# Performance work log

Hardware: AMD Instinct MI355X
Metric: run time of the kernel (lower is better)

## Reference

```python
import jax, jax.numpy as jnp
import numpy as np

N_GLIMPSES = 3
GS = 64          # glimpse_size
IN_C = 3         # input_channels
B, H, W = 64, 512, 512


def get_glimpses(image, loc):
    """Multi-scale glimpse extraction (tf.image.extract_glimpse, centered+normalized)
    followed by antialiased bicubic resize to GS x GS, concatenated on channels."""
    b, h, w, c = image.shape
    max_size = GS * 2 ** (N_GLIMPSES - 1)
    padded = jnp.pad(image, ((0, 0), (max_size, max_size), (max_size, max_size), (0, 0)))
    hp, wp = h + 2 * max_size, w + 2 * max_size
    # normalized+centered offsets: (-1,-1)=upper-left, (1,1)=lower-right of padded image
    center = (loc + 1.0) * 0.5 * jnp.array([hp, wp], dtype=jnp.float32)  # (y, x) per batch
    glimpses = []
    for i in range(N_GLIMPSES):
        s = GS * 2 ** i  # current crop size (python int, static)
        tl = jnp.round(center - 0.5 * s).astype(jnp.int32)
        tl = jnp.clip(tl, 0, jnp.array([hp - s, wp - s], dtype=jnp.int32))

        def slice_one(img, yx):
            return jax.lax.dynamic_slice(img, (yx[0], yx[1], 0), (s, s, c))

        g = jax.vmap(slice_one)(padded, tl)                      # [B, s, s, C]
        g = jax.image.resize(g, (b, GS, GS, c), method='cubic')  # antialiased bicubic
        glimpses.append(g)
    return jnp.concatenate(glimpses, axis=-1)  # [B, GS, GS, N_GLIMPSES*C]


def setup_inputs() -> dict:
    key = jax.random.key(0)
    ks = jax.random.split(key, 10)
    image = jax.random.uniform(ks[0], (B, H, W, IN_C), dtype=jnp.float32)
    loc = jax.random.uniform(ks[1], (B, 2), dtype=jnp.float32, minval=-1.0, maxval=1.0)
    cg = N_GLIMPSES * IN_C
    # conv1_g: full-kernel (GS x GS) valid conv -> 1x1x128
    Wg = jax.random.normal(ks[2], (GS, GS, cg, 128), dtype=jnp.float32) * (1.0 / np.sqrt(GS * GS * cg))
    bg = jnp.zeros((128,), jnp.float32)
    # conv1_l: 1x1 conv on loc [B,1,1,2]
    Wl = jax.random.normal(ks[3], (2, 128), dtype=jnp.float32) * (1.0 / np.sqrt(2.0))
    bl = jnp.zeros((128,), jnp.float32)
    # out: 1x1 conv 128 -> 256
    Wo = jax.random.normal(ks[4], (128, 256), dtype=jnp.float32) * (1.0 / np.sqrt(128.0))
    bo = jnp.zeros((256,), jnp.float32)
    return {"image": image, "loc": loc, "Wg": Wg, "bg": bg, "Wl": Wl, "bl": bl, "Wo": Wo, "bo": bo}


def reference(image, loc, Wg, bg, Wl, bl, Wo, bo):
    glimpses = get_glimpses(image, loc)  # [B, GS, GS, N_GLIMPSES*IN_C]
    # conv1_g with kernel == glimpse size and VALID padding == dense contraction over hwc
    x1 = jax.nn.relu(jnp.einsum('bhwc,hwck->bk', glimpses, Wg) + bg)  # [B,128]
    x2 = jax.nn.relu(loc @ Wl + bl)                                   # [B,128]
    out = jax.nn.relu((x1 + x2) @ Wo + bo)                            # [B,256]
    return out
```

## Files before the change

### kernel.cpp

```cpp
#include <hip/hip_runtime.h>
#include <hip/hip_bf16.h>

#define IMG_H 512
#define IMG_W 512
#define PAD   256
#define HP    1024
#define BATCH 64
#define KTOT  36864
#define KTILE 96
#define NTILES 384
#define TBLK  1152

typedef __attribute__((ext_vector_type(8))) short short8;
typedef __attribute__((ext_vector_type(4))) float f32x4;

__device__ __forceinline__ float keys_cubic(float x) {
  if (x >= 2.0f) return 0.0f;
  if (x >= 1.0f) return ((-0.5f * x + 2.5f) * x - 4.0f) * x + 2.0f;
  return ((1.5f * x - 2.5f) * x) * x + 1.0f;
}

__device__ __forceinline__ int iclamp(int v, int lo, int hi) {
  return min(max(v, lo), hi);
}
__device__ __forceinline__ unsigned short f2bits(float f) {
  __hip_bfloat16 h = __float2bfloat16(f);
  unsigned short s;
  __builtin_memcpy(&s, &h, 2);
  return s;
}

__global__ __launch_bounds__(256) void prep_kernel(
    const float* __restrict__ Wg, unsigned short* __restrict__ Wt,
    float* __restrict__ WT) {
  if (blockIdx.x == TBLK) {
    const int t = threadIdx.x;
    if (t < 64) {
      float sx = ((float)t + 0.5f) * 2.0f - 0.5f;
      int ix0 = (int)ceilf(sx - 4.0f);
      float ws = 0.0f;
#pragma unroll
      for (int tap = 0; tap < 8; ++tap) {
        int i = ix0 + tap;
        float w = (i >= 0 && i < 128) ? keys_cubic(fabsf(sx - (float)i) * 0.5f) : 0.0f;
        WT[t * 9 + tap] = w;
        ws += w;
      }
      WT[t * 9 + 8] = ws;
    } else if (t < 128) {
      const int xo = t - 64;
      float sx = ((float)xo + 0.5f) * 4.0f - 0.5f;
      int ix0 = (int)ceilf(sx - 8.0f);
      float ws = 0.0f;
#pragma unroll
      for (int tap = 0; tap < 16; ++tap) {
        int i = ix0 + tap;
        float w = (i >= 0 && i < 256) ? keys_cubic(fabsf(sx - (float)i) * 0.25f) : 0.0f;
        WT[576 + xo * 17 + tap] = w;
        ws += w;
      }
      WT[576 + xo * 17 + 16] = ws;
    }
    return;
  }

  __shared__ float T[64][68];
  const int tid = threadIdx.x;
  const int kt  = (blockIdx.x % 576) * 64;
  const int nt0 = (blockIdx.x / 576) * 64;
  {
    const int r = tid >> 4, nc = tid & 15;
#pragma unroll
    for (int kk = 0; kk < 4; ++kk) {
      const int k = kk * 16 + r;
      const float4 v = *(const float4*)(Wg + (size_t)(kt + k) * 128 + nt0 + nc * 4);
      *(float4*)(&T[k][nc * 4]) = v;
    }
  }
  __syncthreads();
#pragma unroll
  for (int it = 0; it < 2; ++it) {
    const int item = tid + 256 * it;
    const int n = item & 63, ko = item >> 6;
    short8 o;
#pragma unroll
    for (int j = 0; j < 8; ++j) o[j] = (short)f2bits(T[ko * 8 + j][n]);
    *(short8*)(Wt + (size_t)(nt0 + n) * KTOT + kt + ko * 8) = o;
  }
}

__global__ __launch_bounds__(256) void glimpse_kernel(
    const float* __restrict__ img, const float* __restrict__ loc,
    const float* __restrict__ WT, unsigned short* __restrict__ G) {
  __shared__ __align__(16) float Ws[1664];
  __shared__ float wv1n[8], wv2n[16];
  __shared__ float tmp1[384];
  __shared__ float tmp2[768];
  const int y   = blockIdx.x & 63;
  const int b   = blockIdx.x >> 6;
  const int tid = threadIdx.x;

  {
    const float4* src = (const float4*)WT;
    float4* dst = (float4*)Ws;
    for (int e = tid; e < 416; e += 256) dst[e] = src[e];
  }

  const float cy = (loc[2 * b] + 1.0f) * 0.5f * 1024.0f;
  const float cx = (loc[2 * b + 1] + 1.0f) * 0.5f * 1024.0f;
  const int tly0 = iclamp((int)rintf(cy - 32.0f), 0, HP - 64);
  const int tlx0 = iclamp((int)rintf(cx - 32.0f), 0, HP - 64);
  const int tly1 = iclamp((int)rintf(cy - 64.0f), 0, HP - 128);
  const int tlx1 = iclamp((int)rintf(cx - 64.0f), 0, HP - 128);
  const int tly2 = iclamp((int)rintf(cy - 128.0f), 0, HP - 256);
  const int tlx2 = iclamp((int)rintf(cx - 128.0f), 0, HP - 256);
  const float* imb = img + (size_t)b * (IMG_H * IMG_W * 3);
  unsigned short* Grow = G + ((size_t)b * 64 + y) * (64 * 9);

  if (tid < 192) {
    int x = tid / 3, c = tid - 3 * (tid / 3);
    int py = tly0 + y - PAD, px = tlx0 + x - PAD;
    float v = 0.0f;
    if ((unsigned)py < (unsigned)IMG_H && (unsigned)px < (unsigned)IMG_W)
      v = imb[(py * IMG_W + px) * 3 + c];
    Grow[x * 9 + c] = f2bits(v);
  }
  __syncthreads();

  if (tid < 8) {
    wv1n[tid] = Ws[y * 9 + tid] * (1.0f / Ws[y * 9 + 8]);
  } else if (tid >= 64 && tid < 80) {
    const int t = tid - 64;
    wv2n[t] = Ws[576 + y * 17 + t] * (1.0f / Ws[576 + y * 17 + 16]);
  }
  __syncthreads();

  const float sy1 = ((float)y + 0.5f) * 2.0f - 0.5f;
  const int iy0_1 = (int)ceilf(sy1 - 4.0f);
  const float sy2 = ((float)y + 0.5f) * 4.0f - 0.5f;
  const int iy0_2 = (int)ceilf(sy2 - 8.0f);
  float rw1[8], rw2[16];
#pragma unroll
  for (int t = 0; t < 8; ++t) rw1[t] = wv1n[t];
#pragma unroll
  for (int t = 0; t < 16; ++t) rw2[t] = wv2n[t];

  for (int e = tid; e < 384; e += 256) {
    int x = e / 3, c = e - 3 * (e / 3);
    int px = tlx1 - PAD + x;
    float a = 0.0f;
    if ((unsigned)px < (unsigned)IMG_W) {
      const float* colp = imb + (px * 3 + c);
#pragma unroll
      for (int t = 0; t < 8; ++t) {
        int py = tly1 + iy0_1 + t - PAD;
        if ((unsigned)py < (unsigned)IMG_H)
          a = fmaf(rw1[t], colp[py * (IMG_W * 3)], a);
      }
    }
    tmp1[e] = a;
  }
  for (int e = tid; e < 768; e += 256) {
    int x = e / 3, c = e - 3 * (e / 3);
    int px = tlx2 - PAD + x;
    float a = 0.0f;
    if ((unsigned)px < (unsigned)IMG_W) {
      const float* colp = imb + (px * 3 + c);
#pragma unroll
      for (int t = 0; t < 16; ++t) {
        int py = tly2 + iy0_2 + t - PAD;
        if ((unsigned)py < (unsigned)IMG_H)
          a = fmaf(rw2[t], colp[py * (IMG_W * 3)], a);
      }
    }
    tmp2[e] = a;
  }
  __syncthreads();

  for (int o = tid; o < 384; o += 256) {
    int oo = (o >= 192) ? o - 192 : o;
    int xo = oo / 3, c = oo - 3 * xo;
    if (o < 192) {
      const float* wr = Ws + xo * 9;
      float sx  = ((float)xo + 0.5f) * 2.0f - 0.5f;
      int   ix0 = (int)ceilf(sx - 4.0f);
      float a = 0.0f;
#pragma unroll
      for (int t = 0; t < 8; ++t) {
        int ic = iclamp(ix0 + t, 0, 127);
        a = fmaf(wr[t], tmp1[ic * 3 + c], a);
      }
      Grow[xo * 9 + 3 + c] = f2bits(a / wr[8]);
    } else {
      const float* wr = Ws + 576 + xo * 17;
      float sx  = ((float)xo + 0.5f) * 4.0f - 0.5f;
      int   ix0 = (int)ceilf(sx - 8.0f);
      float a = 0.0f;
#pragma unroll
      for (int t = 0; t < 16; ++t) {
        int ic = iclamp(ix0 + t, 0, 255);
        a = fmaf(wr[t], tmp2[ic * 3 + c], a);
      }
      Grow[xo * 9 + 6 + c] = f2bits(a / wr[16]);
    }
  }
}

__global__ __launch_bounds__(256) void gemm_kernel(
    const unsigned short* __restrict__ G, const unsigned short* __restrict__ Wt,
    float* __restrict__ partials) {
  const int tid  = threadIdx.x;
  const int tile = blockIdx.x;
  const int kt   = tile * KTILE;
  const int lane = tid & 63;
  const int wv   = tid >> 6;
  const int ln   = lane & 15;
  const int q    = lane >> 4;
  const int nb   = wv * 32 + ln;

  f32x4 acc[4][2];
#pragma unroll
  for (int mt = 0; mt < 4; ++mt)
#pragma unroll
    for (int nt = 0; nt < 2; ++nt) {
      acc[mt][nt][0] = 0.f; acc[mt][nt][1] = 0.f;
      acc[mt][nt][2] = 0.f; acc[mt][nt][3] = 0.f;
    }

  const unsigned short* Ab = G + kt + q * 8;
  const unsigned short* Bb = Wt + kt + q * 8;

#pragma unroll
  for (int s = 0; s < KTILE / 32; ++s) {
    short8 af[4];
#pragma unroll
    for (int mt = 0; mt < 4; ++mt)
      af[mt] = *(const short8*)(Ab + (size_t)(mt * 16 + ln) * KTOT + s * 32);
    short8 bf[2];
#pragma unroll
    for (int nt = 0; nt < 2; ++nt)
      bf[nt] = *(const short8*)(Bb + (size_t)(nb + nt * 16) * KTOT + s * 32);
#pragma unroll
    for (int mt = 0; mt < 4; ++mt)
#pragma unroll
      for (int nt = 0; nt < 2; ++nt)
        acc[mt][nt] = __builtin_amdgcn_mfma_f32_16x16x32_bf16(
            af[mt], bf[nt], acc[mt][nt], 0, 0, 0);
  }

#pragma unroll
  for (int mt = 0; mt < 4; ++mt)
#pragma unroll
    for (int nt = 0; nt < 2; ++nt)
#pragma unroll
      for (int i = 0; i < 4; ++i) {
        const int row = mt * 16 + q * 4 + i;
        const int col = nb + nt * 16;
        partials[((size_t)row * NTILES + tile) * 128 + col] = acc[mt][nt][i];
      }
}

__global__ __launch_bounds__(512) void finalize_kernel(
    const float* __restrict__ partials, const float* __restrict__ loc,
    const float* __restrict__ bg, const float* __restrict__ Wl,
    const float* __restrict__ bl, const float* __restrict__ Wo,
    const float* __restrict__ bo, float* __restrict__ out) {
  const int b   = blockIdx.x;
  const int tid = threadIdx.x;

  const float4* base = (const float4*)(partials + (size_t)b * NTILES * 128);
  float4 acc = make_float4(0.f, 0.f, 0.f, 0.f);
#pragma unroll 8
  for (int i = 0; i < 24; ++i) {
    float4 v = base[(size_t)i * 512 + tid];
    acc.x += v.x; acc.y += v.y; acc.z += v.z; acc.w += v.w;
  }

  __shared__ float red[16][128];
  __shared__ float h[128];
  {
    float* r = &red[tid >> 5][(tid & 31) * 4];
    r[0] = acc.x; r[1] = acc.y; r[2] = acc.z; r[3] = acc.w;
  }
  __syncthreads();
  if (tid < 128) {
    float ss = 0.0f;
#pragma unroll
    for (int g = 0; g < 16; ++g) ss += red[g][tid];
    float x1 = fmaxf(ss + bg[tid], 0.0f);
    float x2 = fmaxf(fmaf(loc[2 * b], Wl[tid],
                          fmaf(loc[2 * b + 1], Wl[128 + tid], bl[tid])),
                     0.0f);
    h[tid] = x1 + x2;
  }
  __syncthreads();
  if (tid < 256) {
    const int n = tid;
    float a = bo[n];
#pragma unroll 8
    for (int kk = 0; kk < 128; ++kk) a = fmaf(h[kk], Wo[kk * 256 + n], a);
    out[(size_t)b * 256 + n] = fmaxf(a, 0.0f);
  }
}

extern "C" void kernel_launch(void* const* d_in, const int* in_sizes, int n_in,
                              void* d_out, int out_size, void* d_ws, size_t ws_size,
                              hipStream_t stream) {
  const float* img = (const float*)d_in[0];
  const float* loc = (const float*)d_in[1];
  const float* Wg  = (const float*)d_in[2];
  const float* bg  = (const float*)d_in[3];
  const float* Wl  = (const float*)d_in[4];
  const float* bl  = (const float*)d_in[5];
  const float* Wo  = (const float*)d_in[6];
  const float* bo  = (const float*)d_in[7];
  float* out = (float*)d_out;

  char* ws = (char*)d_ws;
  unsigned short* G = (unsigned short*)ws;
  float* partials   = (float*)(ws + 4718592);
  unsigned short* Wt = (unsigned short*)(ws + 4718592 + 12582912);
  float* WTbl       = (float*)(ws + 4718592 + 12582912 + 9437184);

  prep_kernel<<<TBLK + 1, 256, 0, stream>>>(Wg, Wt, WTbl);
  glimpse_kernel<<<BATCH * 64, 256, 0, stream>>>(img, loc, WTbl, G);
  gemm_kernel<<<NTILES, 256, 0, stream>>>(G, Wt, partials);
  finalize_kernel<<<BATCH, 512, 0, stream>>>(partials, loc, bg, Wl, bl, Wo, bo, out);
}
```

Measured before the change: 317.5 us.

## Merge weight prep and glimpse kernels, retile GEMM split-K across N halves

Fuses the weight transpose/bf16 conversion and glimpse extraction into one launch. Each glimpse block now computes the bicubic tap weights itself instead of reading a precomputed table, which removes a kernel launch and the dependency between the two stages. The GEMM switches to 192-wide K tiles with each block covering one 64-column half of N, giving the same block count with fewer partials. Finalize reduces those partials using 1024 threads. The cost is some redundant weight-table math in every glimpse block and a larger per-block K loop.

```diff
diff --git a/kernel.cpp b/kernel.cpp
--- a/kernel.cpp
+++ b/kernel.cpp
@@ -7,9 +7,10 @@
 #define HP    1024
 #define BATCH 64
 #define KTOT  36864
-#define KTILE 96
-#define NTILES 384
+#define KTILE 192
+#define NKT   192
 #define TBLK  1152
+#define GBLK  4096
 
 typedef __attribute__((ext_vector_type(8))) short short8;
 typedef __attribute__((ext_vector_type(4))) float f32x4;
@@ -30,80 +31,75 @@
   return s;
 }
 
-__global__ __launch_bounds__(256) void prep_kernel(
+__global__ __launch_bounds__(256) void combo_kernel(
+    const float* __restrict__ img, const float* __restrict__ loc,
     const float* __restrict__ Wg, unsigned short* __restrict__ Wt,
-    float* __restrict__ WT) {
-  if (blockIdx.x == TBLK) {
-    const int t = threadIdx.x;
-    if (t < 64) {
-      float sx = ((float)t + 0.5f) * 2.0f - 0.5f;
-      int ix0 = (int)ceilf(sx - 4.0f);
-      float ws = 0.0f;
-#pragma unroll
-      for (int tap = 0; tap < 8; ++tap) {
-        int i = ix0 + tap;
-        float w = (i >= 0 && i < 128) ? keys_cubic(fabsf(sx - (float)i) * 0.5f) : 0.0f;
-        WT[t * 9 + tap] = w;
-        ws += w;
-      }
-      WT[t * 9 + 8] = ws;
-    } else if (t < 128) {
-      const int xo = t - 64;
-      float sx = ((float)xo + 0.5f) * 4.0f - 0.5f;
-      int ix0 = (int)ceilf(sx - 8.0f);
-      float ws = 0.0f;
-#pragma unroll
-      for (int tap = 0; tap < 16; ++tap) {
-        int i = ix0 + tap;
-        float w = (i >= 0 && i < 256) ? keys_cubic(fabsf(sx - (float)i) * 0.25f) : 0.0f;
-        WT[576 + xo * 17 + tap] = w;
-        ws += w;
-      }
-      WT[576 + xo * 17 + 16] = ws;
+    unsigned short* __restrict__ G) {
+  __shared__ __align__(16) float smem[4352];
+  const int tid = threadIdx.x;
+
+  if (blockIdx.x < TBLK) {
+    float (*T)[68] = (float(*)[68])smem;
+    const int bid = blockIdx.x;
+    const int kt  = (bid % 576) * 64;
+    const int nt0 = (bid / 576) * 64;
+    {
+      const int r = tid >> 4, nc = tid & 15;
+#pragma unroll
+      for (int kk = 0; kk < 4; ++kk) {
+        const int k = kk * 16 + r;
+        const float4 v = *(const float4*)(Wg + (size_t)(kt + k) * 128 + nt0 + nc * 4);
+        *(float4*)(&T[k][nc * 4]) = v;
+      }
+    }
+    __syncthreads();
+#pragma unroll
+    for (int it = 0; it < 2; ++it) {
+      const int item = tid + 256 * it;
+      const int n = item & 63, ko = item >> 6;
+      short8 o;
+#pragma unroll
+      for (int j = 0; j < 8; ++j) o[j] = (short)f2bits(T[ko * 8 + j][n]);
+      *(short8*)(Wt + (size_t)(nt0 + n) * KTOT + kt + ko * 8) = o;
     }
     return;
   }
 
-  __shared__ float T[64][68];
-  const int tid = threadIdx.x;
-  const int kt  = (blockIdx.x % 576) * 64;
-  const int nt0 = (blockIdx.x / 576) * 64;
-  {
-    const int r = tid >> 4, nc = tid & 15;
-#pragma unroll
-    for (int kk = 0; kk < 4; ++kk) {
-      const int k = kk * 16 + r;
-      const float4 v = *(const float4*)(Wg + (size_t)(kt + k) * 128 + nt0 + nc * 4);
-      *(float4*)(&T[k][nc * 4]) = v;
-    }
-  }
-  __syncthreads();
-#pragma unroll
-  for (int it = 0; it < 2; ++it) {
-    const int item = tid + 256 * it;
-    const int n = item & 63, ko = item >> 6;
-    short8 o;
-#pragma unroll
-    for (int j = 0; j < 8; ++j) o[j] = (short)f2bits(T[ko * 8 + j][n]);
-    *(short8*)(Wt + (size_t)(nt0 + n) * KTOT + kt + ko * 8) = o;
-  }
-}
-
-__global__ __launch_bounds__(256) void glimpse_kernel(
-    const float* __restrict__ img, const float* __restrict__ loc,
-    const float* __restrict__ WT, unsigned short* __restrict__ G) {
-  __shared__ __align__(16) float Ws[1664];
-  __shared__ float wv1n[8], wv2n[16];
-  __shared__ float tmp1[384];
-  __shared__ float tmp2[768];
-  const int y   = blockIdx.x & 63;
-  const int b   = blockIdx.x >> 6;
-  const int tid = threadIdx.x;
-
-  {
-    const float4* src = (const float4*)WT;
-    float4* dst = (float4*)Ws;
-    for (int e = tid; e < 416; e += 256) dst[e] = src[e];
+  float* Ws   = smem;
+  float* tmp1 = smem + 1664;
+  float* tmp2 = smem + 2048;
+  float* wv1n = smem + 2816;
+  float* wv2n = smem + 2824;
+
+  const int bid = blockIdx.x - TBLK;
+  const int y   = bid & 63;
+  const int b   = bid >> 6;
+
+  if (tid < 64) {
+    float sx = ((float)tid + 0.5f) * 2.0f - 0.5f;
+    int ix0 = (int)ceilf(sx - 4.0f);
+    float ws = 0.0f;
+#pragma unroll
+    for (int tap = 0; tap < 8; ++tap) {
+      int i = ix0 + tap;
+      float w = (i >= 0 && i < 128) ? keys_cubic(fabsf(sx - (float)i) * 0.5f) : 0.0f;
+      Ws[tid * 9 + tap] = w;
+      ws += w;
+    }
+    Ws[tid * 9 + 8] = ws;
+  } else if (tid < 128) {
+    const int xo = tid - 64;
+    float sx = ((float)xo + 0.5f) * 4.0f - 0.5f;
+    int ix0 = (int)ceilf(sx - 8.0f);
+    float ws = 0.0f;
+#pragma unroll
+    for (int tap = 0; tap < 16; ++tap) {
+      int i = ix0 + tap;
+      float w = (i >= 0 && i < 256) ? keys_cubic(fabsf(sx - (float)i) * 0.25f) : 0.0f;
+      Ws[576 + xo * 17 + tap] = w;
+      ws += w;
+    }
+    Ws[576 + xo * 17 + 16] = ws;
   }
 
   const float cy = (loc[2 * b] + 1.0f) * 0.5f * 1024.0f;
@@ -209,26 +205,25 @@
 __global__ __launch_bounds__(256) void gemm_kernel(
     const unsigned short* __restrict__ G, const unsigned short* __restrict__ Wt,
     float* __restrict__ partials) {
-  const int tid  = threadIdx.x;
-  const int tile = blockIdx.x;
-  const int kt   = tile * KTILE;
-  const int lane = tid & 63;
-  const int wv   = tid >> 6;
-  const int ln   = lane & 15;
-  const int q    = lane >> 4;
-  const int nb   = wv * 32 + ln;
-
-  f32x4 acc[4][2];
-#pragma unroll
-  for (int mt = 0; mt < 4; ++mt)
-#pragma unroll
-    for (int nt = 0; nt < 2; ++nt) {
-      acc[mt][nt][0] = 0.f; acc[mt][nt][1] = 0.f;
-      acc[mt][nt][2] = 0.f; acc[mt][nt][3] = 0.f;
-    }
+  const int tid   = threadIdx.x;
+  const int bid   = blockIdx.x;
+  const int ktile = bid >> 1;
+  const int nh    = bid & 1;
+  const int kt    = ktile * KTILE;
+  const int lane  = tid & 63;
+  const int wv    = tid >> 6;
+  const int ln    = lane & 15;
+  const int q     = lane >> 4;
+  const int gcol  = nh * 64 + wv * 16 + ln;
+
+  f32x4 acc[4];
+#pragma unroll
+  for (int mt = 0; mt < 4; ++mt) {
+    acc[mt][0] = 0.f; acc[mt][1] = 0.f; acc[mt][2] = 0.f; acc[mt][3] = 0.f;
+  }
 
   const unsigned short* Ab = G + kt + q * 8;
-  const unsigned short* Bb = Wt + kt + q * 8;
+  const unsigned short* Bb = Wt + (size_t)gcol * KTOT + kt + q * 8;
 
 #pragma unroll
   for (int s = 0; s < KTILE / 32; ++s) {
@@ -236,31 +231,22 @@
 #pragma unroll
     for (int mt = 0; mt < 4; ++mt)
       af[mt] = *(const short8*)(Ab + (size_t)(mt * 16 + ln) * KTOT + s * 32);
-    short8 bf[2];
-#pragma unroll
-    for (int nt = 0; nt < 2; ++nt)
-      bf[nt] = *(const short8*)(Bb + (size_t)(nb + nt * 16) * KTOT + s * 32);
+    const short8 bf = *(const short8*)(Bb + s * 32);
 #pragma unroll
     for (int mt = 0; mt < 4; ++mt)
-#pragma unroll
-      for (int nt = 0; nt < 2; ++nt)
-        acc[mt][nt] = __builtin_amdgcn_mfma_f32_16x16x32_bf16(
-            af[mt], bf[nt], acc[mt][nt], 0, 0, 0);
+      acc[mt] = __builtin_amdgcn_mfma_f32_16x16x32_bf16(af[mt], bf, acc[mt], 0, 0, 0);
   }
 
 #pragma unroll
   for (int mt = 0; mt < 4; ++mt)
 #pragma unroll
-    for (int nt = 0; nt < 2; ++nt)
-#pragma unroll
-      for (int i = 0; i < 4; ++i) {
-        const int row = mt * 16 + q * 4 + i;
-        const int col = nb + nt * 16;
-        partials[((size_t)row * NTILES + tile) * 128 + col] = acc[mt][nt][i];
-      }
-}
-
-__global__ __launch_bounds__(512) void finalize_kernel(
+    for (int i = 0; i < 4; ++i) {
+      const int row = mt * 16 + q * 4 + i;
+      partials[((size_t)row * NKT + ktile) * 128 + gcol] = acc[mt][i];
+    }
+}
+
+__global__ __launch_bounds__(1024) void finalize_kernel(
     const float* __restrict__ partials, const float* __restrict__ loc,
     const float* __restrict__ bg, const float* __restrict__ Wl,
     const float* __restrict__ bl, const float* __restrict__ Wo,
@@ -268,15 +254,15 @@
   const int b   = blockIdx.x;
   const int tid = threadIdx.x;
 
-  const float4* base = (const float4*)(partials + (size_t)b * NTILES * 128);
+  const float4* base = (const float4*)(partials + (size_t)b * NKT * 128);
   float4 acc = make_float4(0.f, 0.f, 0.f, 0.f);
-#pragma unroll 8
-  for (int i = 0; i < 24; ++i) {
-    float4 v = base[(size_t)i * 512 + tid];
+#pragma unroll
+  for (int i = 0; i < 6; ++i) {
+    float4 v = base[(size_t)i * 1024 + tid];
     acc.x += v.x; acc.y += v.y; acc.z += v.z; acc.w += v.w;
   }
 
-  __shared__ float red[16][128];
+  __shared__ float red[32][128];
   __shared__ float h[128];
   {
     float* r = &red[tid >> 5][(tid & 31) * 4];
@@ -286,7 +272,7 @@
   if (tid < 128) {
     float ss = 0.0f;
 #pragma unroll
-    for (int g = 0; g < 16; ++g) ss += red[g][tid];
+    for (int g = 0; g < 32; ++g) ss += red[g][tid];
     float x1 = fmaxf(ss + bg[tid], 0.0f);
     float x2 = fmaxf(fmaf(loc[2 * b], Wl[tid],
                           fmaf(loc[2 * b + 1], Wl[128 + tid], bl[tid])),
@@ -317,13 +303,11 @@
   float* out = (float*)d_out;
 
   char* ws = (char*)d_ws;
-  unsigned short* G = (unsigned short*)ws;
-  float* partials   = (float*)(ws + 4718592);
-  unsigned short* Wt = (unsigned short*)(ws + 4718592 + 12582912);
-  float* WTbl       = (float*)(ws + 4718592 + 12582912 + 9437184);
-
-  prep_kernel<<<TBLK + 1, 256, 0, stream>>>(Wg, Wt, WTbl);
-  glimpse_kernel<<<BATCH * 64, 256, 0, stream>>>(img, loc, WTbl, G);
-  gemm_kernel<<<NTILES, 256, 0, stream>>>(G, Wt, partials);
-  finalize_kernel<<<BATCH, 512, 0, stream>>>(partials, loc, bg, Wl, bl, Wo, bo, out);
-}
+  unsigned short* G  = (unsigned short*)ws;
+  float* partials    = (float*)(ws + 4718592);
+  unsigned short* Wt = (unsigned short*)(ws + 4718592 + 6291456);
+
+  combo_kernel<<<TBLK + GBLK, 256, 0, stream>>>(img, loc, Wg, Wt, G);
+  gemm_kernel<<<NKT * 2, 256, 0, stream>>>(G, Wt, partials);
+  finalize_kernel<<<BATCH, 1024, 0, stream>>>(partials, loc, bg, Wl, bl, Wo, bo, out);
+}
```

Result: no change. 316.4 us (-0.3%).
